# Kernel tuning notes

Measured on AMD Instinct MI355X. Metric: run time of the kernel, lower is better.

## Reference

```python
import jax, jax.numpy as jnp
import numpy as np

B, C = 8192, 10000

def setup_inputs() -> dict:
    key = jax.random.key(0)
    k1, k2, k3 = jax.random.split(key, 3)
    x = jax.random.normal(k1, (B, C), dtype=jnp.float32)
    target = jax.random.randint(k2, (B,), 0, C)
    # soft-label matrix: rows are probability distributions (as produced by update())
    matrix = jax.nn.softmax(jax.random.normal(k3, (C, C), dtype=jnp.float32), axis=-1)
    grad_state = jnp.zeros((C, C), dtype=jnp.float32)
    count = jnp.zeros((C, 1), dtype=jnp.float32)
    return {"x": x, "target": target, "matrix": matrix, "grad_state": grad_state, "count": count}

def reference(x, target, matrix, grad_state, count):
    target = target.reshape(-1)
    logprobs = jax.nn.log_softmax(x, axis=-1)          # [B, C]
    softlabel = matrix[target]                          # gather rows: [B, C]
    loss = jnp.mean(jnp.sum(-softlabel * logprobs, axis=-1))  # reduction='mean'
    # training-branch statistics (detached in original)
    p = jax.nn.softmax(jax.lax.stop_gradient(x), axis=-1)
    pred = jnp.argmax(p, axis=-1)
    correct = (pred == target)                          # [B] bool
    # scatter-add correct probs into per-class rows (replaces python Counter loop)
    add = jax.ops.segment_sum(p * correct[:, None].astype(p.dtype), target, num_segments=C)
    cnt = jax.ops.segment_sum(correct.astype(jnp.float32), target, num_segments=C)[:, None]
    new_grad = grad_state + add
    new_count = count + cnt
    return loss, new_grad, new_count
```

## Files before the change

kernel.cpp:

```cpp
#include <hip/hip_runtime.h>

#define CLS 10000
#define BATCH 8192

__device__ __forceinline__ void combine_ms(float& m, float& s, float om, float os) {
  float nm = fmaxf(m, om);
  s = s * __expf(m - nm) + os * __expf(om - nm);
  m = nm;
}

__global__ __launch_bounds__(256) void rowstats_kernel(
    const float* __restrict__ x, const int* __restrict__ target,
    const float* __restrict__ matrix, float* __restrict__ loss_out,
    float* __restrict__ row_logZ, int* __restrict__ row_correct)
{
  int b = blockIdx.x;
  int t = target[b];
  const float4* xr = (const float4*)(x + (size_t)b * CLS);
  const float4* mr = (const float4*)(matrix + (size_t)t * CLS);

  float m = -3.4e38f, s = 0.f, dot = 0.f;
  float bestv = -3.4e38f;
  int besti = 0x7fffffff;

  for (int i = threadIdx.x; i < CLS / 4; i += 256) {
    float4 xv = xr[i];
    float4 mv = mr[i];
    dot += xv.x * mv.x;
    dot += xv.y * mv.y;
    dot += xv.z * mv.z;
    dot += xv.w * mv.w;
    float vals[4] = {xv.x, xv.y, xv.z, xv.w};
#pragma unroll
    for (int j = 0; j < 4; ++j) {
      float v = vals[j];
      int idx = 4 * i + j;
      if (v > bestv || (v == bestv && idx < besti)) { bestv = v; besti = idx; }
      float nm = fmaxf(m, v);
      s = s * __expf(m - nm) + __expf(v - nm);
      m = nm;
    }
  }

#pragma unroll
  for (int off = 32; off > 0; off >>= 1) {
    float om = __shfl_down(m, off);
    float os = __shfl_down(s, off);
    float od = __shfl_down(dot, off);
    float ov = __shfl_down(bestv, off);
    int   oi = __shfl_down(besti, off);
    combine_ms(m, s, om, os);
    dot += od;
    if (ov > bestv || (ov == bestv && oi < besti)) { bestv = ov; besti = oi; }
  }

  __shared__ float sm[4], ss[4], sd[4], sv[4];
  __shared__ int si[4];
  int wave = threadIdx.x >> 6;
  if ((threadIdx.x & 63) == 0) {
    sm[wave] = m; ss[wave] = s; sd[wave] = dot; sv[wave] = bestv; si[wave] = besti;
  }
  __syncthreads();
  if (threadIdx.x == 0) {
    for (int w = 1; w < 4; ++w) {
      combine_ms(m, s, sm[w], ss[w]);
      dot += sd[w];
      if (sv[w] > bestv || (sv[w] == bestv && si[w] < besti)) { bestv = sv[w]; besti = si[w]; }
    }
    float logZ = m + __logf(s);
    row_logZ[b] = logZ;
    row_correct[b] = (besti == t) ? 1 : 0;
    atomicAdd(loss_out, (logZ - dot) * (1.0f / BATCH));
  }
}

__global__ void copy_kernel(const float* __restrict__ src, float* __restrict__ dst,
                            long long n)
{
  long long stride = (long long)gridDim.x * blockDim.x;
  for (long long i = (long long)blockIdx.x * blockDim.x + threadIdx.x; i < n; i += stride)
    dst[i] = src[i];
}

__global__ __launch_bounds__(256) void scatter_kernel(
    const float* __restrict__ x, const int* __restrict__ target,
    const float* __restrict__ row_logZ, const int* __restrict__ row_correct,
    float* __restrict__ out_grad, float* __restrict__ out_count)
{
  int b = blockIdx.x;
  if (!row_correct[b]) return;
  int t = target[b];
  float lz = row_logZ[b];
  const float* xr = x + (size_t)b * CLS;
  float* gr = out_grad + (size_t)t * CLS;
  for (int c = threadIdx.x; c < CLS; c += 256)
    atomicAdd(&gr[c], __expf(xr[c] - lz));
  if (threadIdx.x == 0) atomicAdd(&out_count[t], 1.0f);
}

extern "C" void kernel_launch(void* const* d_in, const int* in_sizes, int n_in,
                              void* d_out, int out_size, void* d_ws, size_t ws_size,
                              hipStream_t stream)
{
  const float* x          = (const float*)d_in[0];
  const int*   target     = (const int*)d_in[1];
  const float* matrix     = (const float*)d_in[2];
  const float* grad_state = (const float*)d_in[3];
  const float* count      = (const float*)d_in[4];

  float* out       = (float*)d_out;
  float* out_loss  = out;
  float* out_grad  = out + 1;
  float* out_count = out + 1 + (long long)CLS * CLS;

  float* row_logZ    = (float*)d_ws;
  int*   row_correct = (int*)((char*)d_ws + BATCH * sizeof(float));

  hipMemsetAsync(out_loss, 0, sizeof(float), stream);

  rowstats_kernel<<<BATCH, 256, 0, stream>>>(x, target, matrix, out_loss,
                                             row_logZ, row_correct);
  copy_kernel<<<16384, 256, 0, stream>>>(grad_state, out_grad, (long long)CLS * CLS);
  copy_kernel<<<64, 256, 0, stream>>>(count, out_count, (long long)CLS);
  scatter_kernel<<<BATCH, 256, 0, stream>>>(x, target, row_logZ, row_correct,
                                            out_grad, out_count);
}
```

Baseline: 1.121 ms.

## Vectorize grad copy with aligned float4 stores and fold loss reduction into finalize

Replaces the scalar grid-stride copy of the 100M-element grad state with a one-element-per-thread kernel that does four scalar loads and one aligned float4 store into the output, which sits at a 1-float offset. Per-row losses are now written to workspace and summed by a single-block finalize kernel, which also copies count. This removes the memset and the global atomic on the loss. The larger launch grid and the misaligned source reads trade read efficiency for store alignment.

```diff
diff --git a/kernel.cpp b/kernel.cpp
--- a/kernel.cpp
+++ b/kernel.cpp
@@ -2,6 +2,7 @@
 
 #define CLS 10000
 #define BATCH 8192
+#define NGRAD 100000000LL
 
 __device__ __forceinline__ void combine_ms(float& m, float& s, float om, float os) {
   float nm = fmaxf(m, om);
@@ -11,7 +12,7 @@
 
 __global__ __launch_bounds__(256) void rowstats_kernel(
     const float* __restrict__ x, const int* __restrict__ target,
-    const float* __restrict__ matrix, float* __restrict__ loss_out,
+    const float* __restrict__ matrix, float* __restrict__ row_loss,
     float* __restrict__ row_logZ, int* __restrict__ row_correct)
 {
   int b = blockIdx.x;
@@ -70,16 +71,41 @@
     float logZ = m + __logf(s);
     row_logZ[b] = logZ;
     row_correct[b] = (besti == t) ? 1 : 0;
-    atomicAdd(loss_out, (logZ - dot) * (1.0f / BATCH));
+    row_loss[b] = logZ - dot;
   }
 }
 
-__global__ void copy_kernel(const float* __restrict__ src, float* __restrict__ dst,
-                            long long n)
+__global__ __launch_bounds__(256) void copy_grad_kernel(
+    const float* __restrict__ src, float* __restrict__ out)
 {
-  long long stride = (long long)gridDim.x * blockDim.x;
-  for (long long i = (long long)blockIdx.x * blockDim.x + threadIdx.x; i < n; i += stride)
-    dst[i] = src[i];
+  const long long N4 = (NGRAD - 4) / 4;
+  long long k = (long long)blockIdx.x * blockDim.x + threadIdx.x;
+  if (k == 0) {
+    out[1] = src[0]; out[2] = src[1]; out[3] = src[2];
+    out[NGRAD] = src[NGRAD - 1];
+  }
+  if (k < N4) {
+    const float* s = src + 3 + 4 * k;
+    float4 v;
+    v.x = s[0]; v.y = s[1]; v.z = s[2]; v.w = s[3];
+    ((float4*)(out + 4))[k] = v;
+  }
+}
+
+__global__ __launch_bounds__(256) void finalize_kernel(
+    const float* __restrict__ row_loss, const float* __restrict__ count,
+    float* __restrict__ out_loss, float* __restrict__ out_count)
+{
+  float acc = 0.f;
+  for (int i = threadIdx.x; i < BATCH; i += 256) acc += row_loss[i];
+#pragma unroll
+  for (int off = 32; off > 0; off >>= 1) acc += __shfl_down(acc, off);
+  __shared__ float sw[4];
+  if ((threadIdx.x & 63) == 0) sw[threadIdx.x >> 6] = acc;
+  __syncthreads();
+  if (threadIdx.x == 0)
+    out_loss[0] = (sw[0] + sw[1] + sw[2] + sw[3]) * (1.0f / BATCH);
+  for (int c = threadIdx.x; c < CLS; c += 256) out_count[c] = count[c];
 }
 
 __global__ __launch_bounds__(256) void scatter_kernel(
@@ -111,17 +137,18 @@
   float* out       = (float*)d_out;
   float* out_loss  = out;
   float* out_grad  = out + 1;
-  float* out_count = out + 1 + (long long)CLS * CLS;
+  float* out_count = out + 1 + NGRAD;
 
-  float* row_logZ    = (float*)d_ws;
-  int*   row_correct = (int*)((char*)d_ws + BATCH * sizeof(float));
+  float* row_loss    = (float*)d_ws;
+  float* row_logZ    = row_loss + BATCH;
+  int*   row_correct = (int*)(row_logZ + BATCH);
 
-  hipMemsetAsync(out_loss, 0, sizeof(float), stream);
-
-  rowstats_kernel<<<BATCH, 256, 0, stream>>>(x, target, matrix, out_loss,
+  rowstats_kernel<<<BATCH, 256, 0, stream>>>(x, target, matrix, row_loss,
                                              row_logZ, row_correct);
-  copy_kernel<<<16384, 256, 0, stream>>>(grad_state, out_grad, (long long)CLS * CLS);
-  copy_kernel<<<64, 256, 0, stream>>>(count, out_count, (long long)CLS);
+  const long long N4 = (NGRAD - 4) / 4;
+  int copy_blocks = (int)((N4 + 255) / 256);
+  copy_grad_kernel<<<copy_blocks, 256, 0, stream>>>(grad_state, out);
+  finalize_kernel<<<1, 256, 0, stream>>>(row_loss, count, out_loss, out_count);
   scatter_kernel<<<BATCH, 256, 0, stream>>>(x, target, row_logZ, row_correct,
                                             out_grad, out_count);
 }
```

Result: faster. 1.065 ms (-5.0%).
